# Kernel tuning notes

Hardware: AMD Instinct MI355X
Metric: run time of the kernel (lower is better)

The kernel has to match this reference:

```python
import jax, jax.numpy as jnp
import numpy as np

EPS = 1e-5

def _conv(x, w, pad):
    # x: [B,C,H,W] NCHW, w: [O,I,kh,kw] OIHW
    return jax.lax.conv_general_dilated(
        x, w, (1, 1), [(pad, pad), (pad, pad)],
        dimension_numbers=('NCHW', 'OIHW', 'NCHW'))

def _bn(x, g, b, m, v):
    # eval-mode batchnorm folded into scale/shift
    s = g * jax.lax.rsqrt(v + EPS)
    return x * s[None, :, None, None] + (b - m * s)[None, :, None, None]

def _cbr(x, w, g, b, m, v):
    # Convolution block from CornerNet: conv3x3(pad=1, no bias) + BN + ReLU
    return jax.nn.relu(_bn(_conv(x, w, 1), g, b, m, v))


def setup_inputs() -> dict:
    key = jax.random.key(0)
    B, Cin, C, H, W = 4, 256, 256, 128, 128
    kdims = {'up': (C, Cin, 3, 3), 'down': (C, Cin, 3, 3),
             'p': (C, C, 3, 3), 'c1': (C, Cin, 1, 1), 'c2': (C, C, 3, 3)}
    inp = {'x': jax.random.normal(key, (B, Cin, H, W), dtype=jnp.float32)}
    for i, n in enumerate(['up', 'down', 'p', 'c1', 'c2']):
        ks = jax.random.split(jax.random.fold_in(key, i + 1), 5)
        inp['w_' + n] = jax.random.normal(ks[0], kdims[n], dtype=jnp.float32) * 0.02
        inp['g_' + n] = 1.0 + 0.1 * jax.random.normal(ks[1], (C,), dtype=jnp.float32)
        inp['b_' + n] = 0.1 * jax.random.normal(ks[2], (C,), dtype=jnp.float32)
        inp['m_' + n] = 0.1 * jax.random.normal(ks[3], (C,), dtype=jnp.float32)
        inp['v_' + n] = 0.5 + jax.random.uniform(ks[4], (C,), dtype=jnp.float32)
    return inp


def reference(x,
              w_up, g_up, b_up, m_up, v_up,
              w_down, g_down, b_down, m_down, v_down,
              w_p, g_p, b_p, m_p, v_p,
              w_c1, g_c1, b_c1, m_c1, v_c1,
              w_c2, g_c2, b_c2, m_c2, v_c2):
    # up branch: conv-bn-relu then LeftPool (reverse cummax over W) then RightPool (cummax over W)
    up = _cbr(x, w_up, g_up, b_up, m_up, v_up)
    up = jax.lax.cummax(up, axis=3, reverse=True)   # LeftPool
    up = jax.lax.cummax(up, axis=3)                 # RightPool
    # down branch: conv-bn-relu then TopPool (reverse cummax over H) then BottomPool (cummax over H)
    down = _cbr(x, w_down, g_down, b_down, m_down, v_down)
    down = jax.lax.cummax(down, axis=2, reverse=True)  # TopPool
    down = jax.lax.cummax(down, axis=2)                # BottomPool
    # merge path: 3x3 conv + BN on pooled sum
    merge = _bn(_conv(up + down, w_p, 1), g_p, b_p, m_p, v_p)
    # shortcut path: 1x1 conv + BN on input
    bn1 = _bn(_conv(x, w_c1, 0), g_c1, b_c1, m_c1, v_c1)
    relu1 = jax.nn.relu(merge + bn1)
    # output Convolution block
    return _cbr(relu1, w_c2, g_c2, b_c2, m_c2, v_c2)
```

## Files before the change

kernel.cpp:

```cpp
#include <hip/hip_runtime.h>

typedef unsigned short u16;
typedef __attribute__((ext_vector_type(8))) short bf16x8;
typedef __attribute__((ext_vector_type(4))) float f32x4;


__device__ __forceinline__ u16 f2bf(float f) {
  unsigned u = __float_as_uint(f);
  unsigned r = u + 0x7fffu + ((u >> 16) & 1u);
  return (u16)(r >> 16);
}

__device__ __forceinline__ void gll16(const char* g, char* l) {
  __builtin_amdgcn_global_load_lds((const __attribute__((address_space(1))) void*)g,
                                   (__attribute__((address_space(3))) void*)l, 16, 0, 0);
}

__global__ void bn_prep_kernel(const float* __restrict__ g, const float* __restrict__ b,
                               const float* __restrict__ m, const float* __restrict__ v,
                               float* __restrict__ st) {
  int c = threadIdx.x;
  float s = g[c] * rsqrtf(v[c] + 1e-5f);
  st[c] = s;
  st[256 + c] = b[c] - m[c] * s;
}

__global__ void bn_fix_kernel(float* __restrict__ st) {
  int c = threadIdx.x;
  st[2 * 512 + 256 + c] += st[3 * 512 + 256 + c];
  st[3 * 512 + c] = st[3 * 512 + c] / st[2 * 512 + c];
}

__global__ void wprep3_kernel(const float* __restrict__ w, u16* __restrict__ dst) {
  int idx = blockIdx.x * 256 + threadIdx.x;
  int blk = idx >> 12, iu = idx & 4095;
  int co_l = iu >> 5, w32 = iu & 31, slot = w32 >> 3, e = w32 & 7;
  int q = slot ^ ((co_l >> 1) & 3);
  int cohalf = blk / 72, step = blk % 72;
  int outer = step / 12, rr = step % 12, dwi = rr >> 2, kc = rr & 3;
  int half = outer / 3, d = outer % 3;
  int s = d * 3 + dwi;
  int ci = half * 128 + kc * 32 + q * 8 + e;
  int co = cohalf * 128 + co_l;
  dst[idx] = f2bf(w[(co * 256 + ci) * 9 + s]);
}

__global__ void wprep1_kernel(const float* __restrict__ w, u16* __restrict__ dst,
                              const float* __restrict__ ratio) {
  int idx = blockIdx.x * 256 + threadIdx.x;
  int blk = idx >> 12, iu = idx & 4095;
  int co_l = iu >> 5, w32 = iu & 31, slot = w32 >> 3, e = w32 & 7;
  int q = slot ^ ((co_l >> 1) & 3);
  int cohalf = blk >> 3, j = blk & 7;
  int half2 = j >> 2, kc = j & 3;
  int ci = half2 * 128 + kc * 32 + q * 8 + e;
  int co = cohalf * 128 + co_l;
  dst[idx] = f2bf(w[co * 256 + ci] * ratio[co]);
}

__global__ __launch_bounds__(256) void nchw_to_nhwc_kernel(const float* __restrict__ x,
                                                           char* __restrict__ xb) {
  __shared__ __align__(16) u16 tl[128 * 130];
  int bh = blockIdx.x; int b = bh >> 7, h = bh & 127;
  int t = threadIdx.x;
  for (int half = 0; half < 2; ++half) {
    __syncthreads();
    for (int i = 0; i < 64; ++i) {
      int cil = i * 2 + (t >> 7);
      int ci = half * 128 + cil;
      int w = t & 127;
      tl[w * 130 + cil] = f2bf(x[(size_t)((b * 256 + ci) * 128 + h) * 128 + w]);
    }
    __syncthreads();
    char* plane = xb + (size_t)(b * 128 + h) * 65536 + half * 32768;
    for (int i = 0; i < 32; ++i) {
      int w = i * 4 + (t >> 6);
      int c2 = (t & 63) * 2;
      unsigned v = *(const unsigned*)&tl[w * 130 + c2];
      *(unsigned*)(plane + w * 256 + ((c2 * 2) ^ (((w + 1) & 7) << 4))) = v;
    }
  }
}

__device__ __forceinline__ void stage_aw(const char* wA1, const char* wA2, int step,
                                         char* ldsAw, int buf, int coq, int lane) {
  const char* src = (step < 72) ? (wA1 + (size_t)step * 8192)
                                : (wA2 + (size_t)(step - 72) * 8192);
  const char* g = src + coq * 4096 + lane * 16;
  char* dst = ldsAw + buf * 4096 + lane * 16;
#pragma unroll
  for (int k = 0; k < 4; ++k) gll16(g + k * 1024, dst + k * 1024);
}

__device__ __forceinline__ void stage_b(const char* plane, char* ldsB, int t) {
  if (plane) {
    char* dst = ldsB + 256 + t * 16;
    const char* g = plane + t * 16;
#pragma unroll
    for (int r = 0; r < 8; ++r) gll16(g + r * 4096, dst + r * 4096);
  } else {
    int4 z = {0, 0, 0, 0};
#pragma unroll
    for (int r = 0; r < 8; ++r) *(int4*)(ldsB + 256 + r * 4096 + t * 16) = z;
  }
}

__device__ __forceinline__ void zero_acc(f32x4 (&acc)[4][4]) {
  f32x4 z = {0.f, 0.f, 0.f, 0.f};
#pragma unroll
  for (int i = 0; i < 4; ++i)
#pragma unroll
    for (int j = 0; j < 4; ++j) acc[i][j] = z;
}

#define CONV_STEP(WP_ADD, KC)                                                              \
  {                                                                                        \
    if (i + 1 < nsteps) {                                                                  \
      stage_aw(wA1, wA2, i + 1, ldsAw, cur ^ 1, coq, lane);                                \
      asm volatile("s_waitcnt vmcnt(4)" ::: "memory");                                     \
    } else {                                                                               \
      asm volatile("s_waitcnt vmcnt(0)" ::: "memory");                                     \
    }                                                                                      \
    bf16x8 af[4], bf[4];                                                                   \
    const char* lA = ldsAw + cur * 4096;                                                   \
    _Pragma("unroll")                                                                      \
    for (int f = 0; f < 4; ++f) af[f] = *(const bf16x8*)(lA + aOff[f]);                    \
    _Pragma("unroll")                                                                      \
    for (int f = 0; f < 4; ++f) {                                                          \
      int wp = wpb[f] + (WP_ADD);                                                          \
      bf[f] = *(const bf16x8*)(ldsB + wp * 256 + (((KC)*64 + q * 16) ^ ((wp & 7) << 4)));  \
    }                                                                                      \
    __builtin_amdgcn_s_setprio(1);                                                         \
    _Pragma("unroll")                                                                      \
    for (int fm = 0; fm < 4; ++fm)                                                         \
      _Pragma("unroll")                                                                    \
      for (int fn = 0; fn < 4; ++fn)                                                       \
        acc[fm][fn] =                                                                      \
            __builtin_amdgcn_mfma_f32_16x16x32_bf16(af[fm], bf[fn], acc[fm][fn], 0, 0, 0); \
    __builtin_amdgcn_s_setprio(0);                                                         \
    cur ^= 1;                                                                              \
    ++i;                                                                                   \
  }

__device__ __forceinline__ void conv_pipeline(const char* inB1, const char* inB2,
                                              const char* wA1, const char* wA2,
                                              int h, int nsteps, char* lds,
                                              f32x4 (&acc)[4][4]) {
  const int t = threadIdx.x;
  const int wv = t >> 6, lane = t & 63;
  const int lane15 = lane & 15, q = lane >> 4;
  const int coq = wv >> 1, wh = wv & 1;
  char* ldsB = lds;
  char* ldsAw = lds + 33280 + wv * 8192;

  int aOff[4];
#pragma unroll
  for (int f = 0; f < 4; ++f) {
    int ra = f * 16 + lane15;
    aOff[f] = ra * 64 + ((q ^ ((ra >> 1) & 3)) << 4);
  }
  int wpb[4];
#pragma unroll
  for (int f = 0; f < 4; ++f) wpb[f] = wh * 64 + f * 16 + lane15;

  {
    int4 z = {0, 0, 0, 0};
    if (t < 16) *(int4*)(ldsB + t * 16) = z;
    else if (t < 32) *(int4*)(ldsB + 33024 + (t - 16) * 16) = z;
  }

  stage_aw(wA1, wA2, 0, ldsAw, 0, coq, lane);

  int cur = 0, i = 0;
  for (int outer = 0; outer < 6; ++outer) {
    const int half = (outer >= 3) ? 1 : 0;
    const int d = outer - half * 3;
    const int hs = h + d - 1;
    const char* plane = (hs >= 0 && hs < 128)
                            ? inB1 + (size_t)hs * 65536 + (size_t)half * 32768
                            : nullptr;
    asm volatile("s_waitcnt lgkmcnt(0)" ::: "memory");
    __builtin_amdgcn_s_barrier();
    stage_b(plane, ldsB, t);
    asm volatile("s_waitcnt vmcnt(0) lgkmcnt(0)" ::: "memory");
    __builtin_amdgcn_s_barrier();
#pragma unroll
    for (int dwi = 0; dwi < 3; ++dwi)
#pragma unroll
      for (int kc = 0; kc < 4; ++kc) CONV_STEP(dwi, kc)
  }
  if (nsteps > 72) {
    for (int half2 = 0; half2 < 2; ++half2) {
      asm volatile("s_waitcnt lgkmcnt(0)" ::: "memory");
      __builtin_amdgcn_s_barrier();
      stage_b(inB2 + (size_t)h * 65536 + (size_t)half2 * 32768, ldsB, t);
      asm volatile("s_waitcnt vmcnt(0) lgkmcnt(0)" ::: "memory");
      __builtin_amdgcn_s_barrier();
#pragma unroll
      for (int kc = 0; kc < 4; ++kc) CONV_STEP(1, kc)
    }
  }
}

__device__ __forceinline__ void store_pad_relu(f32x4 (&acc)[4][4], const float* __restrict__ st,
                                               int cohalf, int b, int h, char* __restrict__ out) {
  const int t = threadIdx.x, lane = t & 63, wv = t >> 6;
  const int lane15 = lane & 15, q = lane >> 4, coq = wv >> 1, wh = wv & 1;
  char* plane = out + (size_t)(b * 128 + h) * 65536 + cohalf * 32768;
#pragma unroll
  for (int fm = 0; fm < 4; ++fm) {
    int co_l = coq * 64 + fm * 16 + q * 4;
    int co = cohalf * 128 + co_l;
    float ss[4], tt[4];
#pragma unroll
    for (int r = 0; r < 4; ++r) { ss[r] = st[co + r]; tt[r] = st[256 + co + r]; }
#pragma unroll
    for (int fn = 0; fn < 4; ++fn) {
      int w = wh * 64 + fn * 16 + lane15;
      short4 o;
      o.x = (short)f2bf(fmaxf(acc[fm][fn][0] * ss[0] + tt[0], 0.f));
      o.y = (short)f2bf(fmaxf(acc[fm][fn][1] * ss[1] + tt[1], 0.f));
      o.z = (short)f2bf(fmaxf(acc[fm][fn][2] * ss[2] + tt[2], 0.f));
      o.w = (short)f2bf(fmaxf(acc[fm][fn][3] * ss[3] + tt[3], 0.f));
      *(short4*)(plane + w * 256 + ((co_l * 2) ^ (((w + 1) & 7) << 4))) = o;
    }
  }
}

__global__ __launch_bounds__(256, 2) void conv_up_kernel(const char* __restrict__ xb,
                                                         const char* __restrict__ wp,
                                                         const float* __restrict__ st,
                                                         float* __restrict__ rmax) {
  __shared__ __align__(16) char lds[66048];
  int swz = (blockIdx.x & 7) * 64 + (blockIdx.x >> 3);
  int b = swz >> 7, h = swz & 127;
  int cohalf = blockIdx.y;
  const char* wA = wp + (size_t)cohalf * 589824;
  f32x4 acc[4][4];
  zero_acc(acc);
  conv_pipeline(xb + (size_t)b * 8388608, nullptr, wA, wA, h, 72, lds, acc);

  const int t = threadIdx.x, lane = t & 63, wv = t >> 6;
  const int lane15 = lane & 15, q = lane >> 4, coq = wv >> 1, wh = wv & 1;
  float* rlds = (float*)lds;
  __syncthreads();
#pragma unroll
  for (int fm = 0; fm < 4; ++fm) {
    int co_l = coq * 64 + fm * 16 + q * 4;
    int co = cohalf * 128 + co_l;
#pragma unroll
    for (int r = 0; r < 4; ++r) {
      float ss = st[co + r], tt = st[256 + co + r];
      float v = 0.f;
#pragma unroll
      for (int fn = 0; fn < 4; ++fn) v = fmaxf(v, acc[fm][fn][r] * ss + tt);
      v = fmaxf(v, __shfl_xor(v, 1));
      v = fmaxf(v, __shfl_xor(v, 2));
      v = fmaxf(v, __shfl_xor(v, 4));
      v = fmaxf(v, __shfl_xor(v, 8));
      if (lane15 == 0) rlds[wh * 128 + co_l + r] = v;
    }
  }
  __syncthreads();
  if (t < 128)
    rmax[(size_t)(b * 128 + h) * 256 + cohalf * 128 + t] = fmaxf(rlds[t], rlds[128 + t]);
}

__global__ __launch_bounds__(256, 2) void conv_down_kernel(const char* __restrict__ xb,
                                                           const char* __restrict__ wp,
                                                           const float* __restrict__ st,
                                                           char* __restrict__ out) {
  __shared__ __align__(16) char lds[66048];
  int swz = (blockIdx.x & 7) * 64 + (blockIdx.x >> 3);
  int b = swz >> 7, h = swz & 127;
  int cohalf = blockIdx.y;
  const char* wA = wp + (size_t)cohalf * 589824;
  f32x4 acc[4][4];
  zero_acc(acc);
  conv_pipeline(xb + (size_t)b * 8388608, nullptr, wA, wA, h, 72, lds, acc);
  store_pad_relu(acc, st, cohalf, b, h, out);
}

__global__ __launch_bounds__(256) void colmax_kernel(const char* __restrict__ dp,
                                                     float* __restrict__ cmax) {
  int bw = blockIdx.x; int b = bw >> 7, w = bw & 127;
  int c = threadIdx.x;
  size_t base = (size_t)b * 8388608 + (size_t)(c >> 7) * 32768 + w * 256 +
                (((c & 127) * 2) ^ (((w + 1) & 7) << 4));
  float m = 0.f;
  for (int h = 0; h < 128; ++h) {
    u16 raw = *(const u16*)(dp + base + (size_t)h * 65536);
    m = fmaxf(m, __uint_as_float(((unsigned)raw) << 16));
  }
  cmax[(size_t)(b * 128 + w) * 256 + c] = m;
}

__global__ __launch_bounds__(256) void pooled_kernel(const float* __restrict__ rmax,
                                                     const float* __restrict__ cmax,
                                                     char* __restrict__ dp) {
  int bh = blockIdx.x; int b = bh >> 7, h = bh & 127;
  int t = threadIdx.x;
  char* plane = dp + (size_t)(b * 128 + h) * 65536;
  const float* rm = rmax + (size_t)(b * 128 + h) * 256;
#pragma unroll
  for (int it = 0; it < 16; ++it) {
    int id = it * 256 + t;
    int half = id >> 11, rem = id & 2047;
    int w = rem >> 4, slot = rem & 15;
    int c0 = half * 128 + slot * 8;
    const float* cm = cmax + (size_t)(b * 128 + w) * 256 + c0;
    const float* rr = rm + c0;
    u16 e[8];
#pragma unroll
    for (int k = 0; k < 8; ++k) e[k] = f2bf(rr[k] + cm[k]);
    int4 v;
    v.x = (int)(e[0] | ((unsigned)e[1] << 16));
    v.y = (int)(e[2] | ((unsigned)e[3] << 16));
    v.z = (int)(e[4] | ((unsigned)e[5] << 16));
    v.w = (int)(e[6] | ((unsigned)e[7] << 16));
    *(int4*)(plane + half * 32768 + w * 256 + ((slot ^ ((w + 1) & 7)) << 4)) = v;
  }
}

__global__ __launch_bounds__(256, 2) void conv_merge_kernel(const char* __restrict__ dp,
                                                            const char* __restrict__ xb,
                                                            const char* __restrict__ wp_p,
                                                            const char* __restrict__ wp_c1,
                                                            const float* __restrict__ st,
                                                            char* __restrict__ out) {
  __shared__ __align__(16) char lds[66048];
  int swz = (blockIdx.x & 7) * 64 + (blockIdx.x >> 3);
  int b = swz >> 7, h = swz & 127;
  int cohalf = blockIdx.y;
  f32x4 acc[4][4];
  zero_acc(acc);
  conv_pipeline(dp + (size_t)b * 8388608, xb + (size_t)b * 8388608,
                wp_p + (size_t)cohalf * 589824, wp_c1 + (size_t)cohalf * 65536,
                h, 80, lds, acc);
  store_pad_relu(acc, st, cohalf, b, h, out);
}

__global__ __launch_bounds__(256, 2) void conv_c2_kernel(const char* __restrict__ relu1,
                                                         const char* __restrict__ wp,
                                                         const float* __restrict__ st,
                                                         float* __restrict__ out) {
  __shared__ __align__(16) char lds[66048];
  int swz = (blockIdx.x & 7) * 64 + (blockIdx.x >> 3);
  int b = swz >> 7, h = swz & 127;
  int cohalf = blockIdx.y;
  const char* wA = wp + (size_t)cohalf * 589824;
  f32x4 acc[4][4];
  zero_acc(acc);
  conv_pipeline(relu1 + (size_t)b * 8388608, nullptr, wA, wA, h, 72, lds, acc);

  const int t = threadIdx.x, lane = t & 63, wv = t >> 6;
  const int lane15 = lane & 15, q = lane >> 4, coq = wv >> 1, wh = wv & 1;
  float* tl = (float*)lds;
  for (int g = 0; g < 8; ++g) {
    __syncthreads();
    if (coq == (g >> 2)) {
      int fm = g & 3;
      int co_l = coq * 64 + fm * 16 + q * 4;
      int co = cohalf * 128 + co_l;
#pragma unroll
      for (int r = 0; r < 4; ++r) {
        float ss = st[co + r], tt = st[256 + co + r];
#pragma unroll
        for (int fn = 0; fn < 4; ++fn) {
          int w = wh * 64 + fn * 16 + lane15;
          tl[(q * 4 + r) * 132 + w] = fmaxf(acc[fm][fn][r] * ss + tt, 0.f);
        }
      }
    }
    __syncthreads();
    int row = t >> 4, ch = t & 15;
    int co = cohalf * 128 + g * 16 + row;
    float* dst = out + (size_t)((b * 256 + co) * 128 + h) * 128 + ch * 8;
    float4 p0 = *(float4*)&tl[row * 132 + ch * 8];
    float4 p1 = *(float4*)&tl[row * 132 + ch * 8 + 4];
    *(float4*)dst = p0;
    *(float4*)(dst + 4) = p1;
  }
}

extern "C" void kernel_launch(void* const* d_in, const int* in_sizes, int n_in,
                              void* d_out, int out_size, void* d_ws, size_t ws_size,
                              hipStream_t stream) {
  (void)in_sizes; (void)n_in; (void)out_size; (void)ws_size;
  const float* x    = (const float*)d_in[0];
  const float* w_up = (const float*)d_in[1];
  const float* w_dn = (const float*)d_in[6];
  const float* w_p  = (const float*)d_in[11];
  const float* w_c1 = (const float*)d_in[16];
  const float* w_c2 = (const float*)d_in[21];

  char* ws = (char*)d_ws;
  char* xb    = ws;
  char* dp    = ws + 33554432ull;
  char* relu1 = ws + 67108864ull;
  char* wp_up = ws + 100663296ull;
  char* wp_dn = ws + 101842944ull;
  char* wp_p  = ws + 103022592ull;
  char* wp_c2 = ws + 104202240ull;
  char* wp_c1 = ws + 105381888ull;
  float* st   = (float*)(ws + 105512960ull);
  float* rmax = (float*)(ws + 105523200ull);
  float* cmax = (float*)(ws + 106047488ull);

  bn_prep_kernel<<<1, 256, 0, stream>>>((const float*)d_in[2], (const float*)d_in[3],
                                        (const float*)d_in[4], (const float*)d_in[5], st);
  bn_prep_kernel<<<1, 256, 0, stream>>>((const float*)d_in[7], (const float*)d_in[8],
                                        (const float*)d_in[9], (const float*)d_in[10], st + 512);
  bn_prep_kernel<<<1, 256, 0, stream>>>((const float*)d_in[12], (const float*)d_in[13],
                                        (const float*)d_in[14], (const float*)d_in[15], st + 1024);
  bn_prep_kernel<<<1, 256, 0, stream>>>((const float*)d_in[17], (const float*)d_in[18],
                                        (const float*)d_in[19], (const float*)d_in[20], st + 1536);
  bn_prep_kernel<<<1, 256, 0, stream>>>((const float*)d_in[22], (const float*)d_in[23],
                                        (const float*)d_in[24], (const float*)d_in[25], st + 2048);
  bn_fix_kernel<<<1, 256, 0, stream>>>(st);

  wprep3_kernel<<<2304, 256, 0, stream>>>(w_up, (u16*)wp_up);
  wprep3_kernel<<<2304, 256, 0, stream>>>(w_dn, (u16*)wp_dn);
  wprep3_kernel<<<2304, 256, 0, stream>>>(w_p, (u16*)wp_p);
  wprep3_kernel<<<2304, 256, 0, stream>>>(w_c2, (u16*)wp_c2);
  wprep1_kernel<<<256, 256, 0, stream>>>(w_c1, (u16*)wp_c1, st + 1536);

  nchw_to_nhwc_kernel<<<512, 256, 0, stream>>>(x, xb);

  conv_up_kernel<<<dim3(512, 2), 256, 0, stream>>>(xb, wp_up, st, rmax);
  conv_down_kernel<<<dim3(512, 2), 256, 0, stream>>>(xb, wp_dn, st + 512, dp);
  colmax_kernel<<<512, 256, 0, stream>>>(dp, cmax);
  pooled_kernel<<<512, 256, 0, stream>>>(rmax, cmax, dp);
  conv_merge_kernel<<<dim3(512, 2), 256, 0, stream>>>(dp, xb, wp_p, wp_c1, st + 1024, relu1);
  conv_c2_kernel<<<dim3(512, 2), 256, 0, stream>>>(relu1, wp_c2, st + 2048, (float*)d_out);
}
```

Baseline: 397.7 us.

## Compute all 256 output channels per block with shared weight staging

After: 415.1 us. +4.4%, slower.

```diff
diff --git a/kernel.cpp b/kernel.cpp
--- a/kernel.cpp
+++ b/kernel.cpp
@@ -33,28 +33,24 @@
 
 __global__ void wprep3_kernel(const float* __restrict__ w, u16* __restrict__ dst) {
   int idx = blockIdx.x * 256 + threadIdx.x;
-  int blk = idx >> 12, iu = idx & 4095;
-  int co_l = iu >> 5, w32 = iu & 31, slot = w32 >> 3, e = w32 & 7;
-  int q = slot ^ ((co_l >> 1) & 3);
-  int cohalf = blk / 72, step = blk % 72;
+  int step = idx >> 13, iu = idx & 8191;
+  int co = iu >> 5, w32 = iu & 31, slot = w32 >> 3, e = w32 & 7;
+  int q = slot ^ ((co >> 1) & 3);
   int outer = step / 12, rr = step % 12, dwi = rr >> 2, kc = rr & 3;
   int half = outer / 3, d = outer % 3;
   int s = d * 3 + dwi;
   int ci = half * 128 + kc * 32 + q * 8 + e;
-  int co = cohalf * 128 + co_l;
   dst[idx] = f2bf(w[(co * 256 + ci) * 9 + s]);
 }
 
 __global__ void wprep1_kernel(const float* __restrict__ w, u16* __restrict__ dst,
                               const float* __restrict__ ratio) {
   int idx = blockIdx.x * 256 + threadIdx.x;
-  int blk = idx >> 12, iu = idx & 4095;
-  int co_l = iu >> 5, w32 = iu & 31, slot = w32 >> 3, e = w32 & 7;
-  int q = slot ^ ((co_l >> 1) & 3);
-  int cohalf = blk >> 3, j = blk & 7;
-  int half2 = j >> 2, kc = j & 3;
+  int step = idx >> 13, iu = idx & 8191;
+  int co = iu >> 5, w32 = iu & 31, slot = w32 >> 3, e = w32 & 7;
+  int q = slot ^ ((co >> 1) & 3);
+  int half2 = step >> 2, kc = step & 3;
   int ci = half2 * 128 + kc * 32 + q * 8 + e;
-  int co = cohalf * 128 + co_l;
   dst[idx] = f2bf(w[co * 256 + ci] * ratio[co]);
 }
 
@@ -82,14 +78,14 @@
   }
 }
 
-__device__ __forceinline__ void stage_aw(const char* wA1, const char* wA2, int step,
-                                         char* ldsAw, int buf, int coq, int lane) {
-  const char* src = (step < 72) ? (wA1 + (size_t)step * 8192)
-                                : (wA2 + (size_t)(step - 72) * 8192);
-  const char* g = src + coq * 4096 + lane * 16;
-  char* dst = ldsAw + buf * 4096 + lane * 16;
-#pragma unroll
-  for (int k = 0; k < 4; ++k) gll16(g + k * 1024, dst + k * 1024);
+__device__ __forceinline__ void stage_a(const char* wA1, const char* wA2, int step,
+                                        char* ldsA0, int buf, int t) {
+  const char* src = (step < 72) ? (wA1 + (size_t)step * 16384)
+                                : (wA2 + (size_t)(step - 72) * 16384);
+  char* dst = ldsA0 + buf * 16384 + t * 16;
+  const char* g = src + t * 16;
+#pragma unroll
+  for (int k = 0; k < 4; ++k) gll16(g + k * 4096, dst + k * 4096);
 }
 
 __device__ __forceinline__ void stage_b(const char* plane, char* ldsB, int t) {
@@ -105,26 +101,21 @@
   }
 }
 
-__device__ __forceinline__ void zero_acc(f32x4 (&acc)[4][4]) {
+__device__ __forceinline__ void zero_acc(f32x4 (&acc)[8][4]) {
   f32x4 z = {0.f, 0.f, 0.f, 0.f};
 #pragma unroll
-  for (int i = 0; i < 4; ++i)
+  for (int i = 0; i < 8; ++i)
 #pragma unroll
     for (int j = 0; j < 4; ++j) acc[i][j] = z;
 }
 
 #define CONV_STEP(WP_ADD, KC)                                                              \
   {                                                                                        \
-    if (i + 1 < nsteps) {                                                                  \
-      stage_aw(wA1, wA2, i + 1, ldsAw, cur ^ 1, coq, lane);                                \
-      asm volatile("s_waitcnt vmcnt(4)" ::: "memory");                                     \
-    } else {                                                                               \
-      asm volatile("s_waitcnt vmcnt(0)" ::: "memory");                                     \
-    }                                                                                      \
-    bf16x8 af[4], bf[4];                                                                   \
-    const char* lA = ldsAw + cur * 4096;                                                   \
+    if (i + 1 < nsteps) stage_a(wA1, wA2, i + 1, ldsA0, cur ^ 1, t);                       \
+    bf16x8 af[8], bf[4];                                                                   \
+    const char* lA = ldsA0 + cur * 16384;                                                  \
     _Pragma("unroll")                                                                      \
-    for (int f = 0; f < 4; ++f) af[f] = *(const bf16x8*)(lA + aOff[f]);                    \
+    for (int f = 0; f < 8; ++f) af[f] = *(const bf16x8*)(lA + aOff[f]);                    \
     _Pragma("unroll")                                                                      \
     for (int f = 0; f < 4; ++f) {                                                          \
       int wp = wpb[f] + (WP_ADD);                                                          \
@@ -132,12 +123,13 @@
     }                                                                                      \
     __builtin_amdgcn_s_setprio(1);                                                         \
     _Pragma("unroll")                                                                      \
-    for (int fm = 0; fm < 4; ++fm)                                                         \
+    for (int fm = 0; fm < 8; ++fm)                                                         \
       _Pragma("unroll")                                                                    \
       for (int fn = 0; fn < 4; ++fn)                                                       \
         acc[fm][fn] =                                                                      \
             __builtin_amdgcn_mfma_f32_16x16x32_bf16(af[fm], bf[fn], acc[fm][fn], 0, 0, 0); \
     __builtin_amdgcn_s_setprio(0);                                                         \
+    __syncthreads();                                                                       \
     cur ^= 1;                                                                              \
     ++i;                                                                                   \
   }
@@ -145,19 +137,19 @@
 __device__ __forceinline__ void conv_pipeline(const char* inB1, const char* inB2,
                                               const char* wA1, const char* wA2,
                                               int h, int nsteps, char* lds,
-                                              f32x4 (&acc)[4][4]) {
+                                              f32x4 (&acc)[8][4]) {
   const int t = threadIdx.x;
   const int wv = t >> 6, lane = t & 63;
   const int lane15 = lane & 15, q = lane >> 4;
   const int coq = wv >> 1, wh = wv & 1;
   char* ldsB = lds;
-  char* ldsAw = lds + 33280 + wv * 8192;
-
-  int aOff[4];
-#pragma unroll
-  for (int f = 0; f < 4; ++f) {
-    int ra = f * 16 + lane15;
-    aOff[f] = ra * 64 + ((q ^ ((ra >> 1) & 3)) << 4);
+  char* ldsA0 = lds + 33280;
+
+  int aOff[8];
+#pragma unroll
+  for (int f = 0; f < 8; ++f) {
+    int co = coq * 128 + f * 16 + lane15;
+    aOff[f] = co * 64 + ((q ^ ((co >> 1) & 3)) << 4);
   }
   int wpb[4];
 #pragma unroll
@@ -168,8 +160,6 @@
     if (t < 16) *(int4*)(ldsB + t * 16) = z;
     else if (t < 32) *(int4*)(ldsB + 33024 + (t - 16) * 16) = z;
   }
-
-  stage_aw(wA1, wA2, 0, ldsAw, 0, coq, lane);
 
   int cur = 0, i = 0;
   for (int outer = 0; outer < 6; ++outer) {
@@ -179,11 +169,9 @@
     const char* plane = (hs >= 0 && hs < 128)
                             ? inB1 + (size_t)hs * 65536 + (size_t)half * 32768
                             : nullptr;
-    asm volatile("s_waitcnt lgkmcnt(0)" ::: "memory");
-    __builtin_amdgcn_s_barrier();
     stage_b(plane, ldsB, t);
-    asm volatile("s_waitcnt vmcnt(0) lgkmcnt(0)" ::: "memory");
-    __builtin_amdgcn_s_barrier();
+    if (outer == 0) stage_a(wA1, wA2, 0, ldsA0, 0, t);
+    __syncthreads();
 #pragma unroll
     for (int dwi = 0; dwi < 3; ++dwi)
 #pragma unroll
@@ -191,26 +179,22 @@
   }
   if (nsteps > 72) {
     for (int half2 = 0; half2 < 2; ++half2) {
-      asm volatile("s_waitcnt lgkmcnt(0)" ::: "memory");
-      __builtin_amdgcn_s_barrier();
       stage_b(inB2 + (size_t)h * 65536 + (size_t)half2 * 32768, ldsB, t);
-      asm volatile("s_waitcnt vmcnt(0) lgkmcnt(0)" ::: "memory");
-      __builtin_amdgcn_s_barrier();
+      __syncthreads();
 #pragma unroll
       for (int kc = 0; kc < 4; ++kc) CONV_STEP(1, kc)
     }
   }
 }
 
-__device__ __forceinline__ void store_pad_relu(f32x4 (&acc)[4][4], const float* __restrict__ st,
-                                               int cohalf, int b, int h, char* __restrict__ out) {
+__device__ __forceinline__ void store_pad_relu(f32x4 (&acc)[8][4], const float* __restrict__ st,
+                                               int b, int h, char* __restrict__ out) {
   const int t = threadIdx.x, lane = t & 63, wv = t >> 6;
   const int lane15 = lane & 15, q = lane >> 4, coq = wv >> 1, wh = wv & 1;
-  char* plane = out + (size_t)(b * 128 + h) * 65536 + cohalf * 32768;
-#pragma unroll
-  for (int fm = 0; fm < 4; ++fm) {
-    int co_l = coq * 64 + fm * 16 + q * 4;
-    int co = cohalf * 128 + co_l;
+  char* plane = out + (size_t)(b * 128 + h) * 65536;
+#pragma unroll
+  for (int fm = 0; fm < 8; ++fm) {
+    int co = coq * 128 + fm * 16 + q * 4;
     float ss[4], tt[4];
 #pragma unroll
     for (int r = 0; r < 4; ++r) { ss[r] = st[co + r]; tt[r] = st[256 + co + r]; }
@@ -222,7 +206,7 @@
       o.y = (short)f2bf(fmaxf(acc[fm][fn][1] * ss[1] + tt[1], 0.f));
       o.z = (short)f2bf(fmaxf(acc[fm][fn][2] * ss[2] + tt[2], 0.f));
       o.w = (short)f2bf(fmaxf(acc[fm][fn][3] * ss[3] + tt[3], 0.f));
-      *(short4*)(plane + w * 256 + ((co_l * 2) ^ (((w + 1) & 7) << 4))) = o;
+      *(short4*)(plane + (co >> 7) * 32768 + w * 256 + (((co & 127) * 2) ^ (((w + 1) & 7) << 4))) = o;
     }
   }
 }
@@ -234,20 +218,17 @@
   __shared__ __align__(16) char lds[66048];
   int swz = (blockIdx.x & 7) * 64 + (blockIdx.x >> 3);
   int b = swz >> 7, h = swz & 127;
-  int cohalf = blockIdx.y;
-  const char* wA = wp + (size_t)cohalf * 589824;
-  f32x4 acc[4][4];
+  f32x4 acc[8][4];
   zero_acc(acc);
-  conv_pipeline(xb + (size_t)b * 8388608, nullptr, wA, wA, h, 72, lds, acc);
+  conv_pipeline(xb + (size_t)b * 8388608, nullptr, wp, wp, h, 72, lds, acc);
 
   const int t = threadIdx.x, lane = t & 63, wv = t >> 6;
   const int lane15 = lane & 15, q = lane >> 4, coq = wv >> 1, wh = wv & 1;
   float* rlds = (float*)lds;
   __syncthreads();
 #pragma unroll
-  for (int fm = 0; fm < 4; ++fm) {
-    int co_l = coq * 64 + fm * 16 + q * 4;
-    int co = cohalf * 128 + co_l;
+  for (int fm = 0; fm < 8; ++fm) {
+    int co = coq * 128 + fm * 16 + q * 4;
 #pragma unroll
     for (int r = 0; r < 4; ++r) {
       float ss = st[co + r], tt = st[256 + co + r];
@@ -258,12 +239,12 @@
       v = fmaxf(v, __shfl_xor(v, 2));
       v = fmaxf(v, __shfl_xor(v, 4));
       v = fmaxf(v, __shfl_xor(v, 8));
-      if (lane15 == 0) rlds[wh * 128 + co_l + r] = v;
+      if (lane15 == 0) rlds[wh * 256 + co + r] = v;
     }
   }
   __syncthreads();
-  if (t < 128)
-    rmax[(size_t)(b * 128 + h) * 256 + cohalf * 128 + t] = fmaxf(rlds[t], rlds[128 + t]);
+  if (t < 256)
+    rmax[(size_t)(b * 128 + h) * 256 + t] = fmaxf(rlds[t], rlds[256 + t]);
 }
 
 __global__ __launch_bounds__(256, 2) void conv_down_kernel(const char* __restrict__ xb,
@@ -273,12 +254,10 @@
   __shared__ __align__(16) char lds[66048];
   int swz = (blockIdx.x & 7) * 64 + (blockIdx.x >> 3);
   int b = swz >> 7, h = swz & 127;
-  int cohalf = blockIdx.y;
-  const char* wA = wp + (size_t)cohalf * 589824;
-  f32x4 acc[4][4];
+  f32x4 acc[8][4];
   zero_acc(acc);
-  conv_pipeline(xb + (size_t)b * 8388608, nullptr, wA, wA, h, 72, lds, acc);
-  store_pad_relu(acc, st, cohalf, b, h, out);
+  conv_pipeline(xb + (size_t)b * 8388608, nullptr, wp, wp, h, 72, lds, acc);
+  store_pad_relu(acc, st, b, h, out);
 }
 
 __global__ __launch_bounds__(256) void colmax_kernel(const char* __restrict__ dp,
@@ -331,13 +310,11 @@
   __shared__ __align__(16) char lds[66048];
   int swz = (blockIdx.x & 7) * 64 + (blockIdx.x >> 3);
   int b = swz >> 7, h = swz & 127;
-  int cohalf = blockIdx.y;
-  f32x4 acc[4][4];
+  f32x4 acc[8][4];
   zero_acc(acc);
-  conv_pipeline(dp + (size_t)b * 8388608, xb + (size_t)b * 8388608,
-                wp_p + (size_t)cohalf * 589824, wp_c1 + (size_t)cohalf * 65536,
+  conv_pipeline(dp + (size_t)b * 8388608, xb + (size_t)b * 8388608, wp_p, wp_c1,
                 h, 80, lds, acc);
-  store_pad_relu(acc, st, cohalf, b, h, out);
+  store_pad_relu(acc, st, b, h, out);
 }
 
 __global__ __launch_bounds__(256, 2) void conv_c2_kernel(const char* __restrict__ relu1,
@@ -347,21 +324,18 @@
   __shared__ __align__(16) char lds[66048];
   int swz = (blockIdx.x & 7) * 64 + (blockIdx.x >> 3);
   int b = swz >> 7, h = swz & 127;
-  int cohalf = blockIdx.y;
-  const char* wA = wp + (size_t)cohalf * 589824;
-  f32x4 acc[4][4];
+  f32x4 acc[8][4];
   zero_acc(acc);
-  conv_pipeline(relu1 + (size_t)b * 8388608, nullptr, wA, wA, h, 72, lds, acc);
+  conv_pipeline(relu1 + (size_t)b * 8388608, nullptr, wp, wp, h, 72, lds, acc);
 
   const int t = threadIdx.x, lane = t & 63, wv = t >> 6;
   const int lane15 = lane & 15, q = lane >> 4, coq = wv >> 1, wh = wv & 1;
   float* tl = (float*)lds;
-  for (int g = 0; g < 8; ++g) {
+  for (int g = 0; g < 16; ++g) {
     __syncthreads();
-    if (coq == (g >> 2)) {
-      int fm = g & 3;
-      int co_l = coq * 64 + fm * 16 + q * 4;
-      int co = cohalf * 128 + co_l;
+    if (coq == (g >> 3)) {
+      int fm = g & 7;
+      int co = coq * 128 + fm * 16 + q * 4;
 #pragma unroll
       for (int r = 0; r < 4; ++r) {
         float ss = st[co + r], tt = st[256 + co + r];
@@ -374,7 +348,7 @@
     }
     __syncthreads();
     int row = t >> 4, ch = t & 15;
-    int co = cohalf * 128 + g * 16 + row;
+    int co = g * 16 + row;
     float* dst = out + (size_t)((b * 256 + co) * 128 + h) * 128 + ch * 8;
     float4 p0 = *(float4*)&tl[row * 132 + ch * 8];
     float4 p1 = *(float4*)&tl[row * 132 + ch * 8 + 4];
@@ -427,10 +401,10 @@
 
   nchw_to_nhwc_kernel<<<512, 256, 0, stream>>>(x, xb);
 
-  conv_up_kernel<<<dim3(512, 2), 256, 0, stream>>>(xb, wp_up, st, rmax);
-  conv_down_kernel<<<dim3(512, 2), 256, 0, stream>>>(xb, wp_dn, st + 512, dp);
+  conv_up_kernel<<<512, 256, 0, stream>>>(xb, wp_up, st, rmax);
+  conv_down_kernel<<<512, 256, 0, stream>>>(xb, wp_dn, st + 512, dp);
   colmax_kernel<<<512, 256, 0, stream>>>(dp, cmax);
   pooled_kernel<<<512, 256, 0, stream>>>(rmax, cmax, dp);
-  conv_merge_kernel<<<dim3(512, 2), 256, 0, stream>>>(dp, xb, wp_p, wp_c1, st + 1024, relu1);
-  conv_c2_kernel<<<dim3(512, 2), 256, 0, stream>>>(relu1, wp_c2, st + 2048, (float*)d_out);
-}
+  conv_merge_kernel<<<512, 256, 0, stream>>>(dp, xb, wp_p, wp_c1, st + 1024, relu1);
+  conv_c2_kernel<<<512, 256, 0, stream>>>(relu1, wp_c2, st + 2048, (float*)d_out);
+}
```
